# Performance work log

Measured on AMD Instinct MI355X. Metric: run time of the kernel, lower is better.

The kernel has to match this reference:

```python
import jax, jax.numpy as jnp
import numpy as np

HEADS = 16
EPS = 1e-6


def setup_inputs() -> dict:
    key = jax.random.key(0)
    k1, k2, k3 = jax.random.split(key, 3)
    B, N, C = 4, 4096, 1024
    x = jax.random.normal(k1, (B, N, C), dtype=jnp.float32)
    w_qkv = jax.random.normal(k2, (3 * C, C), dtype=jnp.float32) * (C ** -0.5)
    w_out = jax.random.normal(k3, (C, C), dtype=jnp.float32) * (C ** -0.5)
    b_out = jnp.zeros((C,), dtype=jnp.float32)
    return {"x": x, "w_qkv": w_qkv, "w_out": w_out, "b_out": b_out}


def reference(x, w_qkv, w_out, b_out):
    B, N, C = x.shape
    H = HEADS
    D = C // H
    scale = D ** -0.25

    qkv = x @ w_qkv.T  # [B, N, 3C]
    q, k, v = jnp.split(qkv, 3, axis=-1)

    def heads(t):  # [B, N, C] -> [B, H, N, D]
        return t.reshape(B, N, H, D).transpose(0, 2, 1, 3)

    q, k, v = heads(q), heads(k), heads(v)

    feat = lambda t: jax.nn.elu(t) + 1.0
    q = feat(q) * scale
    k = feat(k) * scale

    kv = jnp.einsum('bhnd,bhne->bhde', k, v)      # [B, H, D, D]
    out = jnp.einsum('bhnd,bhde->bhne', q, kv)    # [B, H, N, D]
    k_sum = k.sum(axis=2)                          # [B, H, D]
    denom = jnp.einsum('bhnd,bhd->bhn', q, k_sum)  # [B, H, N]
    out = out / (denom[..., None] + EPS)

    out = out.transpose(0, 2, 1, 3).reshape(B, N, C)
    return out @ w_out.T + b_out
```

## Files before the change

### kernel.cpp

```cpp
#include <hip/hip_runtime.h>
#include <hip/hip_bf16.h>
#include <cmath>


typedef __bf16 bf16_t;
typedef __attribute__((ext_vector_type(8))) __bf16 bf16x8;
typedef __attribute__((ext_vector_type(4))) __bf16 bf16x4;
typedef __attribute__((ext_vector_type(4))) float f32x4;
typedef __attribute__((ext_vector_type(8))) float f32x8;

#define MFMA16(a, b, c) __builtin_amdgcn_mfma_f32_16x16x32_bf16((a), (b), (c), 0, 0, 0)

#define LDS_PITCH 72

__device__ __forceinline__ f32x4 zf4() { f32x4 z; z[0] = 0.f; z[1] = 0.f; z[2] = 0.f; z[3] = 0.f; return z; }

__device__ __forceinline__ float feat(float x) { return x > 0.f ? x + 1.f : expf(x); }

__device__ __forceinline__ void gld_lds16(const bf16_t* src, bf16_t* dst)
{
    __builtin_amdgcn_global_load_lds(
        (__attribute__((address_space(1))) void*)const_cast<bf16_t*>(src),
        (__attribute__((address_space(3))) void*)dst, 16, 0, 0);
}

template <int NR>
__device__ __forceinline__ void stage_async(const bf16_t* g, int ld, bf16_t* lds, int tid)
{
    const int w = tid >> 6, l = tid & 63;
    constexpr int CALLS = NR >> 5;
#pragma unroll
    for (int p = 0; p < CALLS; ++p) {
        const int chunk = w * CALLS + p;
        const int gidx = chunk * 64 + l;
        const int row = gidx >> 3;
        const int cp = gidx & 7;
        const int c = cp ^ (row & 7);
        gld_lds16(g + row * ld + c * 8, lds + chunk * 512);
    }
}

__device__ __forceinline__ bf16x8 read_frag_sw(const bf16_t* lds, int row, int cg)
{
    const int sw = cg ^ (row & 7);
    return *(const bf16x8*)(lds + row * 64 + sw * 8);
}

template <int NR>
__device__ __forceinline__ void stage_bf16(const bf16_t* g, int ld, bf16_t* lds, int tid)
{
#pragma unroll
    for (int p = 0; p < NR * 8 / 256; ++p) {
        const int gidx = p * 256 + tid;
        const int row = gidx >> 3;
        const int cp = gidx & 7;
        *(bf16x8*)(lds + row * LDS_PITCH + cp * 8) = *(const bf16x8*)(g + row * ld + cp * 8);
    }
}

__device__ __forceinline__ bf16x8 read_frag(const bf16_t* lds, int row, int cg)
{
    return *(const bf16x8*)(lds + row * LDS_PITCH + cg * 8);
}

__global__ __launch_bounds__(256) void cvt3_kernel(
    const float* __restrict__ x, bf16_t* __restrict__ xb,
    const float* __restrict__ wq, bf16_t* __restrict__ wqb,
    const float* __restrict__ wo, bf16_t* __restrict__ wob)
{
    const int bid = blockIdx.x;
    const float* src;
    bf16_t* dst;
    int base;
    if (bid < 8192)      { src = x;  dst = xb;  base = bid; }
    else if (bid < 9728) { src = wq; dst = wqb; base = bid - 8192; }
    else                 { src = wo; dst = wob; base = bid - 9728; }
    const size_t idx = ((size_t)base * 256 + threadIdx.x) * 8;
    f32x8 f = *(const f32x8*)(src + idx);
    bf16x8 v;
#pragma unroll
    for (int t = 0; t < 8; ++t) v[t] = (bf16_t)f[t];
    *(bf16x8*)(dst + idx) = v;
}

template <int MODE>
__global__ __launch_bounds__(256, 3) void gemm_bt_kernel(
    const bf16_t* __restrict__ A, const bf16_t* __restrict__ B, int K,
    void* __restrict__ out0, bf16_t* __restrict__ out1, bf16_t* __restrict__ out2,
    const float* __restrict__ bias)
{
    __shared__ __align__(16) bf16_t As[128 * 64];
    __shared__ __align__(16) bf16_t Bs[128 * 64];
    const int tid = threadIdx.x;
    const int l = tid & 63, w = tid >> 6;
    const int wm = w >> 1, wn = w & 1;
    const int quad = l >> 4, r16 = l & 15;
    const int m0 = blockIdx.y * 128;
    const int n0 = blockIdx.x * 128;

    f32x4 acc[4][4];
#pragma unroll
    for (int i = 0; i < 4; ++i)
#pragma unroll
        for (int j = 0; j < 4; ++j) acc[i][j] = zf4();

    const bf16_t* Ab = A + (size_t)m0 * K;
    const bf16_t* Bb = B + (size_t)n0 * K;

    for (int k0 = 0; k0 < K; k0 += 64) {
        stage_async<128>(Ab + k0, K, As, tid);
        stage_async<128>(Bb + k0, K, Bs, tid);
        __syncthreads();
#pragma unroll
        for (int ks = 0; ks < 2; ++ks) {
            const int cg = ks * 4 + quad;
            bf16x8 af[4], bfr[4];
#pragma unroll
            for (int i = 0; i < 4; ++i) af[i] = read_frag_sw(As, wm * 64 + i * 16 + r16, cg);
#pragma unroll
            for (int j = 0; j < 4; ++j) bfr[j] = read_frag_sw(Bs, wn * 64 + j * 16 + r16, cg);
#pragma unroll
            for (int i = 0; i < 4; ++i)
#pragma unroll
                for (int j = 0; j < 4; ++j)
                    acc[i][j] = MFMA16(af[i], bfr[j], acc[i][j]);
        }
        __syncthreads();
    }

    const float scale = 0.3535533905932738f;
#pragma unroll
    for (int i = 0; i < 4; ++i) {
        const int mbase = m0 + wm * 64 + i * 16 + quad * 4;
#pragma unroll
        for (int j = 0; j < 4; ++j) {
            const int col = n0 + wn * 64 + j * 16 + r16;
            if (MODE == 1) {
                float* yp = (float*)out0;
                const float bb = bias[col];
#pragma unroll
                for (int r = 0; r < 4; ++r)
                    yp[(size_t)(mbase + r) * 1024 + col] = acc[i][j][r] + bb;
            } else {
                const int part = col >> 10;
                const int cc = col & 1023;
                const int hh = (mbase >> 12) * 16 + (cc >> 6);
                const int d = cc & 63;
                const int ntok = mbase & 4095;
                if (part == 0) {
                    bf16_t* qp = (bf16_t*)out0 + ((size_t)hh * 4096 + ntok) * 64 + d;
#pragma unroll
                    for (int r = 0; r < 4; ++r)
                        qp[(size_t)r * 64] = (bf16_t)(feat(acc[i][j][r]) * scale);
                } else {
                    bf16_t* tp = (part == 1 ? out1 : out2) + ((size_t)hh * 64 + d) * 4096 + ntok;
                    bf16x4 pk;
#pragma unroll
                    for (int r = 0; r < 4; ++r) {
                        float v = acc[i][j][r];
                        if (part == 1) v = feat(v) * scale;
                        pk[r] = (bf16_t)v;
                    }
                    *(bf16x4*)tp = pk;
                }
            }
        }
    }
}

__global__ __launch_bounds__(256, 2) void kv_partial_kernel(
    const bf16_t* __restrict__ KT, const bf16_t* __restrict__ VT,
    float* __restrict__ kvp, float* __restrict__ ksp_out)
{
    __shared__ __align__(16) bf16_t Ks[64 * LDS_PITCH];
    __shared__ __align__(16) bf16_t Vs[64 * LDS_PITCH];
    const int tid = threadIdx.x;
    const int l = tid & 63, w = tid >> 6;
    const int quad = l >> 4, r16 = l & 15;
    const int hh = blockIdx.x;
    const int ksp = blockIdx.y;
    const bf16_t* kb = KT + (size_t)hh * 64 * 4096 + ksp * 512;
    const bf16_t* vb = VT + (size_t)hh * 64 * 4096 + ksp * 512;

    bf16x8 ones;
#pragma unroll
    for (int t = 0; t < 8; ++t) ones[t] = (bf16_t)1.0f;

    f32x4 acc[4], accks[4];
#pragma unroll
    for (int j = 0; j < 4; ++j) { acc[j] = zf4(); accks[j] = zf4(); }

    for (int k0 = 0; k0 < 512; k0 += 64) {
        stage_bf16<64>(kb + k0, 4096, Ks, tid);
        stage_bf16<64>(vb + k0, 4096, Vs, tid);
        __syncthreads();
#pragma unroll
        for (int ks = 0; ks < 2; ++ks) {
            const int cg = ks * 4 + quad;
            bf16x8 af = read_frag(Vs, w * 16 + r16, cg);
            bf16x8 bk[4];
#pragma unroll
            for (int j = 0; j < 4; ++j) bk[j] = read_frag(Ks, j * 16 + r16, cg);
#pragma unroll
            for (int j = 0; j < 4; ++j) acc[j] = MFMA16(af, bk[j], acc[j]);
            if (w == 0) {
#pragma unroll
                for (int j = 0; j < 4; ++j) accks[j] = MFMA16(ones, bk[j], accks[j]);
            }
        }
        __syncthreads();
    }

    float* ob = kvp + (size_t)(hh * 8 + ksp) * 4096;
    const int ebase = w * 16 + quad * 4;
#pragma unroll
    for (int j = 0; j < 4; ++j)
#pragma unroll
        for (int r = 0; r < 4; ++r)
            ob[(ebase + r) * 64 + j * 16 + r16] = acc[j][r];

    if (w == 0 && quad == 0) {
        float* kso = ksp_out + (size_t)(hh * 8 + ksp) * 64;
#pragma unroll
        for (int j = 0; j < 4; ++j) kso[j * 16 + r16] = accks[j][0];
    }
}

__global__ __launch_bounds__(256) void kvfix_kernel(
    const float* __restrict__ kvp, const float* __restrict__ ksp,
    bf16_t* __restrict__ kvb, bf16_t* __restrict__ ksumb)
{
    const int hh = blockIdx.x, c = blockIdx.y, t = threadIdx.x;
    const float* base = kvp + (size_t)hh * 8 * 4096 + c * 1024 + t * 4;
    f32x4 s = *(const f32x4*)base;
#pragma unroll
    for (int p = 1; p < 8; ++p) s += *(const f32x4*)(base + (size_t)p * 4096);
    bf16x4 o;
#pragma unroll
    for (int r = 0; r < 4; ++r) o[r] = (bf16_t)s[r];
    *(bf16x4*)(kvb + (size_t)hh * 4096 + c * 1024 + t * 4) = o;

    if (c == 0 && t < 64) {
        const float* kb = ksp + (size_t)hh * 8 * 64 + t;
        float ks = 0.f;
#pragma unroll
        for (int p = 0; p < 8; ++p) ks += kb[(size_t)p * 64];
        ksumb[(size_t)hh * 64 + t] = (bf16_t)ks;
    }
}

__global__ __launch_bounds__(256, 2) void attn_out_kernel(
    const bf16_t* __restrict__ Q, const bf16_t* __restrict__ kvb, const bf16_t* __restrict__ ksumb,
    bf16_t* __restrict__ att)
{
    __shared__ __align__(16) bf16_t kvT[64 * LDS_PITCH];
    __shared__ __align__(16) bf16_t ksb[64];
    const int tid = threadIdx.x;
    const int l = tid & 63, w = tid >> 6;
    const int quad = l >> 4, r16 = l & 15;
    const int hh = blockIdx.x;
    const int b = hh >> 4, h = hh & 15;
    const int mt = blockIdx.y;

    {
        const int e = tid >> 2, d0 = (tid & 3) * 16;
        const bf16_t* kvbh = kvb + (size_t)hh * 4096;
        *(bf16x8*)(kvT + e * LDS_PITCH + d0)     = *(const bf16x8*)(kvbh + e * 64 + d0);
        *(bf16x8*)(kvT + e * LDS_PITCH + d0 + 8) = *(const bf16x8*)(kvbh + e * 64 + d0 + 8);
        if (tid < 64) ksb[tid] = ksumb[(size_t)hh * 64 + tid];
    }
    __syncthreads();

    f32x4 acc[4][4];
    f32x4 dacc[4];
#pragma unroll
    for (int i = 0; i < 4; ++i) {
        dacc[i] = zf4();
#pragma unroll
        for (int j = 0; j < 4; ++j) acc[i][j] = zf4();
    }

    const int m0w = mt * 256 + w * 64;
    const bf16_t* qb = Q + (size_t)hh * 4096 * 64;
#pragma unroll
    for (int ks = 0; ks < 2; ++ks) {
        bf16x8 kf = *(const bf16x8*)(ksb + ks * 32 + quad * 8);
        if (r16 != 0) {
#pragma unroll
            for (int t = 0; t < 8; ++t) kf[t] = (bf16_t)0.f;
        }
        bf16x8 bfr[4];
#pragma unroll
        for (int j = 0; j < 4; ++j)
            bfr[j] = *(const bf16x8*)(kvT + (j * 16 + r16) * LDS_PITCH + ks * 32 + quad * 8);
#pragma unroll
        for (int i = 0; i < 4; ++i) {
            const bf16_t* qp = qb + (size_t)(m0w + i * 16 + r16) * 64 + ks * 32 + quad * 8;
            const bf16x8 af = *(const bf16x8*)qp;
            dacc[i] = MFMA16(af, kf, dacc[i]);
#pragma unroll
            for (int j = 0; j < 4; ++j) acc[i][j] = MFMA16(af, bfr[j], acc[i][j]);
        }
    }

#pragma unroll
    for (int i = 0; i < 4; ++i) {
        float den[4];
#pragma unroll
        for (int r = 0; r < 4; ++r)
            den[r] = __shfl(dacc[i][r], l & 48) + 1e-6f;
#pragma unroll
        for (int j = 0; j < 4; ++j) {
            const size_t colb = (size_t)h * 64 + j * 16 + r16;
#pragma unroll
            for (int r = 0; r < 4; ++r) {
                const int ntok = m0w + i * 16 + quad * 4 + r;
                att[((size_t)b * 4096 + ntok) * 1024 + colb] = (bf16_t)(acc[i][j][r] / den[r]);
            }
        }
    }
}

extern "C" void kernel_launch(void* const* d_in, const int* in_sizes, int n_in,
                              void* d_out, int out_size, void* d_ws, size_t ws_size,
                              hipStream_t stream)
{
    const float* x    = (const float*)d_in[0];
    const float* wqkv = (const float*)d_in[1];
    const float* wout = (const float*)d_in[2];
    const float* bout = (const float*)d_in[3];
    float* y = (float*)d_out;

    char* ws = (char*)d_ws;
    bf16_t* xb    = (bf16_t*)ws;
    bf16_t* wqkvb = (bf16_t*)(ws + (size_t)32 * 1048576);
    bf16_t* woutb = (bf16_t*)(ws + (size_t)38 * 1048576);
    bf16_t* Q     = (bf16_t*)(ws + (size_t)40 * 1048576);
    bf16_t* KT    = (bf16_t*)(ws + (size_t)72 * 1048576);
    bf16_t* VT    = (bf16_t*)(ws + (size_t)104 * 1048576);
    float* kvp    = (float*)ws;
    float* ksp    = (float*)(ws + (size_t)8 * 1048576);
    bf16_t* kvb   = (bf16_t*)(ws + (size_t)9 * 1048576);
    bf16_t* ksumb = (bf16_t*)(ws + (size_t)10 * 1048576);
    bf16_t* att   = KT;

    cvt3_kernel<<<10240, 256, 0, stream>>>(x, xb, wqkv, wqkvb, wout, woutb);

    gemm_bt_kernel<0><<<dim3(24, 128), 256, 0, stream>>>(xb, wqkvb, 1024, Q, KT, VT, nullptr);
    kv_partial_kernel<<<dim3(64, 8), 256, 0, stream>>>(KT, VT, kvp, ksp);
    kvfix_kernel<<<dim3(64, 4), 256, 0, stream>>>(kvp, ksp, kvb, ksumb);
    attn_out_kernel<<<dim3(64, 16), 256, 0, stream>>>(Q, kvb, ksumb, att);
    gemm_bt_kernel<1><<<dim3(8, 128), 256, 0, stream>>>(att, woutb, 1024, y, nullptr, nullptr, bout);
}
```

Measured before the change: 328.9 us.

## Fuse KV partial reduction into attn_out, async-swizzle KV staging, raise GEMM occupancy

Removes the kvfix kernel and has each attn_out block sum the 8 fp32 KV partials and k-sum partials itself before writing them to LDS. This saves a launch and an intermediate bf16 buffer, but every one of the 16 blocks per head now repeats the same reduction. kv_partial now stages through the swizzled global_load_lds path instead of padded register copies. The GEMM launch bound is raised to 4 blocks per CU, which may raise register pressure and cause spills.

```diff
diff --git a/kernel.cpp b/kernel.cpp
--- a/kernel.cpp
+++ b/kernel.cpp
@@ -44,23 +44,6 @@
 {
     const int sw = cg ^ (row & 7);
     return *(const bf16x8*)(lds + row * 64 + sw * 8);
-}
-
-template <int NR>
-__device__ __forceinline__ void stage_bf16(const bf16_t* g, int ld, bf16_t* lds, int tid)
-{
-#pragma unroll
-    for (int p = 0; p < NR * 8 / 256; ++p) {
-        const int gidx = p * 256 + tid;
-        const int row = gidx >> 3;
-        const int cp = gidx & 7;
-        *(bf16x8*)(lds + row * LDS_PITCH + cp * 8) = *(const bf16x8*)(g + row * ld + cp * 8);
-    }
-}
-
-__device__ __forceinline__ bf16x8 read_frag(const bf16_t* lds, int row, int cg)
-{
-    return *(const bf16x8*)(lds + row * LDS_PITCH + cg * 8);
 }
 
 __global__ __launch_bounds__(256) void cvt3_kernel(
@@ -84,7 +67,7 @@
 }
 
 template <int MODE>
-__global__ __launch_bounds__(256, 3) void gemm_bt_kernel(
+__global__ __launch_bounds__(256, 4) void gemm_bt_kernel(
     const bf16_t* __restrict__ A, const bf16_t* __restrict__ B, int K,
     void* __restrict__ out0, bf16_t* __restrict__ out1, bf16_t* __restrict__ out2,
     const float* __restrict__ bias)
@@ -172,8 +155,8 @@
     const bf16_t* __restrict__ KT, const bf16_t* __restrict__ VT,
     float* __restrict__ kvp, float* __restrict__ ksp_out)
 {
-    __shared__ __align__(16) bf16_t Ks[64 * LDS_PITCH];
-    __shared__ __align__(16) bf16_t Vs[64 * LDS_PITCH];
+    __shared__ __align__(16) bf16_t Ks[64 * 64];
+    __shared__ __align__(16) bf16_t Vs[64 * 64];
     const int tid = threadIdx.x;
     const int l = tid & 63, w = tid >> 6;
     const int quad = l >> 4, r16 = l & 15;
@@ -191,16 +174,16 @@
     for (int j = 0; j < 4; ++j) { acc[j] = zf4(); accks[j] = zf4(); }
 
     for (int k0 = 0; k0 < 512; k0 += 64) {
-        stage_bf16<64>(kb + k0, 4096, Ks, tid);
-        stage_bf16<64>(vb + k0, 4096, Vs, tid);
+        stage_async<64>(kb + k0, 4096, Ks, tid);
+        stage_async<64>(vb + k0, 4096, Vs, tid);
         __syncthreads();
 #pragma unroll
         for (int ks = 0; ks < 2; ++ks) {
             const int cg = ks * 4 + quad;
-            bf16x8 af = read_frag(Vs, w * 16 + r16, cg);
+            bf16x8 af = read_frag_sw(Vs, w * 16 + r16, cg);
             bf16x8 bk[4];
 #pragma unroll
-            for (int j = 0; j < 4; ++j) bk[j] = read_frag(Ks, j * 16 + r16, cg);
+            for (int j = 0; j < 4; ++j) bk[j] = read_frag_sw(Ks, j * 16 + r16, cg);
 #pragma unroll
             for (int j = 0; j < 4; ++j) acc[j] = MFMA16(af, bk[j], acc[j]);
             if (w == 0) {
@@ -226,31 +209,8 @@
     }
 }
 
-__global__ __launch_bounds__(256) void kvfix_kernel(
-    const float* __restrict__ kvp, const float* __restrict__ ksp,
-    bf16_t* __restrict__ kvb, bf16_t* __restrict__ ksumb)
-{
-    const int hh = blockIdx.x, c = blockIdx.y, t = threadIdx.x;
-    const float* base = kvp + (size_t)hh * 8 * 4096 + c * 1024 + t * 4;
-    f32x4 s = *(const f32x4*)base;
-#pragma unroll
-    for (int p = 1; p < 8; ++p) s += *(const f32x4*)(base + (size_t)p * 4096);
-    bf16x4 o;
-#pragma unroll
-    for (int r = 0; r < 4; ++r) o[r] = (bf16_t)s[r];
-    *(bf16x4*)(kvb + (size_t)hh * 4096 + c * 1024 + t * 4) = o;
-
-    if (c == 0 && t < 64) {
-        const float* kb = ksp + (size_t)hh * 8 * 64 + t;
-        float ks = 0.f;
-#pragma unroll
-        for (int p = 0; p < 8; ++p) ks += kb[(size_t)p * 64];
-        ksumb[(size_t)hh * 64 + t] = (bf16_t)ks;
-    }
-}
-
 __global__ __launch_bounds__(256, 2) void attn_out_kernel(
-    const bf16_t* __restrict__ Q, const bf16_t* __restrict__ kvb, const bf16_t* __restrict__ ksumb,
+    const bf16_t* __restrict__ Q, const float* __restrict__ kvp, const float* __restrict__ ksp,
     bf16_t* __restrict__ att)
 {
     __shared__ __align__(16) bf16_t kvT[64 * LDS_PITCH];
@@ -264,10 +224,29 @@
 
     {
         const int e = tid >> 2, d0 = (tid & 3) * 16;
-        const bf16_t* kvbh = kvb + (size_t)hh * 4096;
-        *(bf16x8*)(kvT + e * LDS_PITCH + d0)     = *(const bf16x8*)(kvbh + e * 64 + d0);
-        *(bf16x8*)(kvT + e * LDS_PITCH + d0 + 8) = *(const bf16x8*)(kvbh + e * 64 + d0 + 8);
-        if (tid < 64) ksb[tid] = ksumb[(size_t)hh * 64 + tid];
+        const float* kvph = kvp + (size_t)hh * 8 * 4096 + e * 64 + d0;
+        f32x4 s[4];
+#pragma unroll
+        for (int q4 = 0; q4 < 4; ++q4) s[q4] = *(const f32x4*)(kvph + q4 * 4);
+#pragma unroll
+        for (int p = 1; p < 8; ++p)
+#pragma unroll
+            for (int q4 = 0; q4 < 4; ++q4) s[q4] += *(const f32x4*)(kvph + p * 4096 + q4 * 4);
+        bf16x8 o0, o1;
+#pragma unroll
+        for (int r = 0; r < 4; ++r) {
+            o0[r] = (bf16_t)s[0][r]; o0[4 + r] = (bf16_t)s[1][r];
+            o1[r] = (bf16_t)s[2][r]; o1[4 + r] = (bf16_t)s[3][r];
+        }
+        *(bf16x8*)(kvT + e * LDS_PITCH + d0)     = o0;
+        *(bf16x8*)(kvT + e * LDS_PITCH + d0 + 8) = o1;
+        if (tid < 64) {
+            const float* kp = ksp + (size_t)hh * 8 * 64 + tid;
+            float ks = 0.f;
+#pragma unroll
+            for (int p = 0; p < 8; ++p) ks += kp[p * 64];
+            ksb[tid] = (bf16_t)ks;
+        }
     }
     __syncthreads();
 
@@ -340,15 +319,12 @@
     bf16_t* VT    = (bf16_t*)(ws + (size_t)104 * 1048576);
     float* kvp    = (float*)ws;
     float* ksp    = (float*)(ws + (size_t)8 * 1048576);
-    bf16_t* kvb   = (bf16_t*)(ws + (size_t)9 * 1048576);
-    bf16_t* ksumb = (bf16_t*)(ws + (size_t)10 * 1048576);
     bf16_t* att   = KT;
 
     cvt3_kernel<<<10240, 256, 0, stream>>>(x, xb, wqkv, wqkvb, wout, woutb);
 
     gemm_bt_kernel<0><<<dim3(24, 128), 256, 0, stream>>>(xb, wqkvb, 1024, Q, KT, VT, nullptr);
     kv_partial_kernel<<<dim3(64, 8), 256, 0, stream>>>(KT, VT, kvp, ksp);
-    kvfix_kernel<<<dim3(64, 4), 256, 0, stream>>>(kvp, ksp, kvb, ksumb);
-    attn_out_kernel<<<dim3(64, 16), 256, 0, stream>>>(Q, kvb, ksumb, att);
+    attn_out_kernel<<<dim3(64, 16), 256, 0, stream>>>(Q, kvp, ksp, att);
     gemm_bt_kernel<1><<<dim3(8, 128), 256, 0, stream>>>(att, woutb, 1024, y, nullptr, nullptr, bout);
 }
```

Result: no change. 331.4 us (+0.8%).
